# Optimization experiments

Hardware: AMD Instinct MI355X
Metric: run time of the kernel (lower is better)

## Reference

```python
import jax, jax.numpy as jnp
import numpy as np

B, L = 128, 5000
D_MODEL, N_LAYERS, D_STATE, D_INNER, D_CONV, DT_RANK = 8, 4, 16, 16, 3, 1
HID, N_CLASSES = 64, 230


def setup_inputs():
    key = jax.random.key(0)
    ks = iter(jax.random.split(key, 32))
    nrm = lambda shape, s=0.02: jax.random.normal(next(ks), shape, jnp.float32) * s
    return {
        "x": jax.random.uniform(next(ks), (B, L), jnp.float32),
        "idx": jnp.arange(L, dtype=jnp.int32),
        "embed": nrm((L, D_MODEL), 1.0),
        "norm_w": jnp.ones((N_LAYERS, D_MODEL), jnp.float32),
        "in_proj_w": nrm((N_LAYERS, 2 * D_INNER, D_MODEL), 0.2),
        "conv_w": nrm((N_LAYERS, D_INNER, 1, D_CONV), 0.3),
        "conv_b": nrm((N_LAYERS, D_INNER)),
        "x_proj_w": nrm((N_LAYERS, DT_RANK + 2 * D_STATE, D_INNER), 0.2),
        "dt_proj_w": nrm((N_LAYERS, D_INNER, DT_RANK), 0.5),
        "dt_proj_b": nrm((N_LAYERS, D_INNER), 0.1),
        "A_log": jnp.broadcast_to(jnp.log(jnp.arange(1., D_STATE + 1.)), (N_LAYERS, D_INNER, D_STATE)).astype(jnp.float32),
        "Dp": jnp.ones((N_LAYERS, D_INNER), jnp.float32),
        "out_proj_w": nrm((N_LAYERS, D_MODEL, D_INNER), 0.2),
        "c1_w": nrm((HID, D_MODEL, 3), 0.2), "c1_b": nrm((HID,)),
        "c2_w": nrm((HID, HID, 3), 0.1), "c2_b": nrm((HID,)),
        "c3_w": nrm((HID, HID, 3), 0.1), "c3_b": nrm((HID,)),
        "fc_w": nrm((N_CLASSES, HID), 0.1), "fc_b": jnp.zeros((N_CLASSES,), jnp.float32),
    }


def _conv1d(x, w, b, pad, groups=1):
    # x: [B, C, L], w: [O, I/groups, K]
    y = jax.lax.conv_general_dilated(x, w, (1,), [pad], dimension_numbers=("NCH", "OIH", "NCH"), feature_group_count=groups)
    return y + b[None, :, None]


def _rmsnorm(x, w, eps=1e-5):
    return x * jax.lax.rsqrt(jnp.mean(x * x, -1, keepdims=True) + eps) * w


def _selective_scan(u, delta, A, Bm, Cm, Dv):
    # u, delta: [B, L, ED]; A: [ED, N]; Bm, Cm: [B, L, N]
    dA = jnp.exp(delta[..., None] * A)                       # [B, L, ED, N]
    dBu = delta[..., None] * Bm[:, :, None, :] * u[..., None]  # [B, L, ED, N]

    def step(h, t):
        dA_t, dBu_t, c_t = t
        h = dA_t * h + dBu_t                                  # [B, ED, N]
        return h, jnp.einsum("ben,bn->be", h, c_t)

    h0 = jnp.zeros((dA.shape[0], dA.shape[2], dA.shape[3]), u.dtype)
    _, ys = jax.lax.scan(step, h0, (dA.swapaxes(0, 1), dBu.swapaxes(0, 1), Cm.swapaxes(0, 1)))
    return ys.swapaxes(0, 1) + Dv * u


def reference(x, idx, embed, norm_w, in_proj_w, conv_w, conv_b, x_proj_w, dt_proj_w, dt_proj_b, A_log, Dp, out_proj_w, c1_w, c1_b, c2_w, c2_b, c3_w, c3_b, fc_w, fc_b):
    # embedding(idx) broadcast over batch, gated by intensities x
    f = embed[idx][None, :, :] * x[:, :, None]                # [B, L, D_MODEL]
    for l in range(N_LAYERS):
        xn = _rmsnorm(f, norm_w[l])
        xz = xn @ in_proj_w[l].T                              # [B, L, 2*ED]
        xc, z = xz[..., :D_INNER], xz[..., D_INNER:]
        xc = _conv1d(xc.swapaxes(1, 2), conv_w[l], conv_b[l], (D_CONV - 1, 0), D_INNER).swapaxes(1, 2)
        xc = jax.nn.silu(xc)
        dbc = xc @ x_proj_w[l].T                              # [B, L, dt_rank+2N]
        delta = jax.nn.softplus(dbc[..., :DT_RANK] @ dt_proj_w[l].T + dt_proj_b[l])
        Bm = dbc[..., DT_RANK:DT_RANK + D_STATE]
        Cm = dbc[..., DT_RANK + D_STATE:]
        y = _selective_scan(xc, delta, -jnp.exp(A_log[l]), Bm, Cm, Dp[l])
        f = (y * jax.nn.silu(z)) @ out_proj_w[l].T + f        # residual
    feat = f.swapaxes(1, 2)                                   # [B, D_MODEL, L]
    h = jax.nn.relu(_conv1d(feat, c1_w, c1_b, (1, 1)))
    r = jax.nn.relu(_conv1d(h, c2_w, c2_b, (1, 1)))
    r = _conv1d(r, c3_w, c3_b, (1, 1))
    h = jax.nn.relu(h + r)                                    # residual conv block
    pooled = h.mean(-1)                                       # [B, HID]
    return pooled @ fc_w.T + fc_b                             # [B, N_CLASSES]
```

## Files before the change

kernel.cpp:

```cpp
#include <hip/hip_runtime.h>
#include <math.h>

#define B 128
#define L 5000
#define NL 4
#define NCH 50
#define LC 100
#define ST 50
#define HT 128

typedef __attribute__((ext_vector_type(8))) short bf16x8;
typedef __attribute__((ext_vector_type(4))) short short4v;
typedef __attribute__((ext_vector_type(4))) float f32x4;

__device__ __forceinline__ float sigmoidf_(float x){ return 1.f/(1.f+__expf(-x)); }
__device__ __forceinline__ float siluf_(float x){ return x*sigmoidf_(x); }
__device__ __forceinline__ float softplusf_(float x){ return fmaxf(x,0.f) + log1pf(__expf(-fabsf(x))); }
__device__ __forceinline__ short bfc_(float x){
  union { float f; unsigned u; } v; v.f = x;
  unsigned r = v.u + 0x7fffu + ((v.u >> 16) & 1u);
  return (short)(r >> 16);
}
__device__ __forceinline__ float b2f_(short s){
  union { unsigned u; float f; } v; v.u = ((unsigned)(unsigned short)s) << 16;
  return v.f;
}
#define SW(row, col) (((row)<<6) + ((col) ^ (((row)&7)<<3)))

__global__ void k_embed(const float* __restrict__ x, const int* __restrict__ idx,
                        const float* __restrict__ embed, float* __restrict__ f){
  int gid = blockIdx.x*256 + threadIdx.x;
  if (gid >= B*L) return;
  int t = gid % L;
  float xv = x[gid];
  const float* er = embed + (size_t)idx[t]*8;
  float4 e0 = *(const float4*)(er);
  float4 e1 = *(const float4*)(er+4);
  *(float4*)(f + (size_t)gid*8)   = make_float4(e0.x*xv, e0.y*xv, e0.z*xv, e0.w*xv);
  *(float4*)(f + (size_t)gid*8+4) = make_float4(e1.x*xv, e1.y*xv, e1.z*xv, e1.w*xv);
}

__global__ __launch_bounds__(256,4) void k_l1(const float* __restrict__ fin,
    const float* __restrict__ norm_w, const float* __restrict__ in_proj,
    const float* __restrict__ conv_w, const float* __restrict__ conv_b,
    const float* __restrict__ x_proj, const float* __restrict__ dt_w,
    const float* __restrict__ dt_b, const float* __restrict__ A_log,
    float* __restrict__ Sc, float* __restrict__ Pc,
    float2* __restrict__ duA, float2* __restrict__ BCA, float* __restrict__ szA){
  __shared__ float fsub[52][8], rn[52];
  __shared__ float uL[ST][17];
  __shared__ float2 duL[ST][16];
  __shared__ float BLs[ST][17];
  __shared__ float dbc0[ST];
  int tid = threadIdx.x, ch = blockIdx.x, b = blockIdx.y;
  int e = tid>>4, n = tid&15;
  int ct = tid&15;
  float ipnw_c[8], ipnwz_c[8], cwc[3];
  #pragma unroll
  for (int d=0;d<8;d++){
    ipnw_c[d]  = in_proj[ct*8+d]*norm_w[d];
    ipnwz_c[d] = in_proj[(16+ct)*8+d]*norm_w[d];
  }
  #pragma unroll
  for (int k=0;k<3;k++) cwc[k] = conv_w[ct*3+k];
  float cbc = conv_b[ct];
  float xp0_c = x_proj[ct];
  float xpB_r[16], xpC_r[16];
  #pragma unroll
  for (int k=0;k<16;k++){
    xpB_r[k] = x_proj[(1+ct)*16+k];
    xpC_r[k] = x_proj[(17+ct)*16+k];
  }
  float dtw_e = dt_w[ct], dtb_e = dt_b[ct];
  float a = -__expf(A_log[e*16+n]);
  float h = 0.f, dsum = 0.f;
  int t00 = ch*LC;
  for (int sub=0; sub<LC/ST; sub++){
    int ts = t00 + sub*ST;
    __syncthreads();
    for (int i=tid;i<104;i+=256){ int r=i>>1, half=i&1; int t=ts-2+r;
      *(float4*)&fsub[r][half*4] = (t>=0) ? *(const float4*)&fin[((size_t)b*L+t)*8+half*4]
                                          : make_float4(0.f,0.f,0.f,0.f); }
    __syncthreads();
    if (tid < 52){ float ss=0.f;
      #pragma unroll
      for (int d=0;d<8;d++){ float v=fsub[tid][d]; ss += v*v; }
      rn[tid] = rsqrtf(ss*0.125f + 1e-5f); }
    __syncthreads();
    for (int i=tid;i<ST*16;i+=256){ int j=i>>4;
      float acc = cbc;
      #pragma unroll
      for (int kk=0;kk<3;kk++){
        int r = j + kk;
        float dot=0.f;
        #pragma unroll
        for (int d=0;d<8;d++) dot += ipnw_c[d]*fsub[r][d];
        acc += cwc[kk]*(dot*rn[r]);
      }
      float uv = siluf_(acc);
      uL[j][ct] = uv;
      int r2 = j + 2;
      float dz=0.f;
      #pragma unroll
      for (int d=0;d<8;d++) dz += ipnwz_c[d]*fsub[r2][d];
      szA[((size_t)b*L + ts + j)*16 + ct] = siluf_(dz*rn[r2]);
      float pp = xp0_c*uv;
      pp += __shfl_xor(pp, 1, 64);
      pp += __shfl_xor(pp, 2, 64);
      pp += __shfl_xor(pp, 4, 64);
      pp += __shfl_xor(pp, 8, 64);
      if (ct == 0) dbc0[j] = pp;
    }
    __syncthreads();
    for (int i=tid;i<ST*16;i+=256){ int j=i>>4;
      float accB=0.f, accC=0.f;
      #pragma unroll
      for (int c=0;c<16;c++){
        float uv2 = uL[j][c];
        accB += xpB_r[c]*uv2;
        accC += xpC_r[c]*uv2;
      }
      BLs[j][ct] = accB;
      float dd = softplusf_(dbc0[j]*dtw_e + dtb_e);
      float uv = uL[j][ct];
      duL[j][ct] = make_float2(dd, dd*uv);
      size_t gi = ((size_t)b*L + ts + j)*16 + ct;
      BCA[gi] = make_float2(accB, accC);
      duA[gi] = make_float2(dd, uv);
    }
    __syncthreads();
    for (int j=0;j<ST;j++){
      float2 du = duL[j][e];
      float bb = BLs[j][n];
      h = __expf(du.x*a)*h + du.y*bb;
      dsum += du.x;
    }
  }
  size_t o = ((size_t)b*NCH + ch)*256 + tid;
  Sc[o] = h;
  Pc[o] = __expf(a*dsum);
}

__global__ __launch_bounds__(256,4) void k_l3(const float* __restrict__ fin, float* __restrict__ fout,
    const float* __restrict__ A_log, const float* __restrict__ Dp,
    const float* __restrict__ Sc, const float* __restrict__ Pc,
    const float* __restrict__ ow,
    const float2* __restrict__ duA, const float2* __restrict__ BCA,
    const float* __restrict__ szA){
  __shared__ float2 duL[ST*16], BCL[ST*16];
  __shared__ float uLs[ST*16], szL[ST*16], yL[ST*16];
  __shared__ float hcL[10*320];
  __shared__ float s_owp[8*17], s_De[16];
  int tid = threadIdx.x, ch = blockIdx.x, b = blockIdx.y;
  int e = tid>>4, n = tid&15;
  int dt8 = tid&7;
  float a = -__expf(A_log[e*16+n]);
  if (tid < 128) s_owp[(tid>>4)*17 + (tid&15)] = ow[tid];
  if (tid < 16) s_De[tid] = Dp[tid];
  float h = 0.f;
  for (int c2=0; c2<ch; c2++){
    size_t o = ((size_t)b*NCH + c2)*256 + tid;
    h = Pc[o]*h + Sc[o];
  }
  int t00 = ch*LC;
  for (int sub=0; sub<LC/ST; sub++){
    int ts = t00 + sub*ST;
    __syncthreads();
    const f32x4* duG = (const f32x4*)(duA + ((size_t)b*L + ts)*16);
    const f32x4* bcG = (const f32x4*)(BCA + ((size_t)b*L + ts)*16);
    for (int i=tid;i<400;i+=256){
      f32x4 v = duG[i];
      int bidx = i*2;
      duL[bidx]   = make_float2(v[0], v[0]*v[1]);
      duL[bidx+1] = make_float2(v[2], v[2]*v[3]);
      uLs[bidx]   = v[1];
      uLs[bidx+1] = v[3];
      f32x4 wv = bcG[i];
      BCL[bidx]   = make_float2(wv[0], wv[1]);
      BCL[bidx+1] = make_float2(wv[2], wv[3]);
    }
    const f32x4* szG = (const f32x4*)(szA + ((size_t)b*L + ts)*16);
    for (int i=tid;i<200;i+=256){
      *(f32x4*)&szL[i*4] = szG[i];
    }
    __syncthreads();
    for (int q=0; q<ST/10; q++){
      #pragma unroll
      for (int j2=0; j2<10; j2++){
        int j = q*10 + j2;
        float2 du = duL[j*16+e];
        float2 bc = BCL[j*16+n];
        h = __expf(du.x*a)*h + du.y*bc.x;
        hcL[j2*320 + e*20 + n] = h*bc.y;
      }
      __syncthreads();
      if (tid < 160){
        int jj = tid>>4, ee = tid&15;
        int j = q*10 + jj;
        const f32x4* hp = (const f32x4*)&hcL[jj*320 + ee*20];
        f32x4 p0 = hp[0], p1 = hp[1], p2 = hp[2], p3 = hp[3];
        float s = ((p0[0]+p0[1])+(p0[2]+p0[3])) + ((p1[0]+p1[1])+(p1[2]+p1[3]))
                + ((p2[0]+p2[1])+(p2[2]+p2[3])) + ((p3[0]+p3[1])+(p3[2]+p3[3]));
        yL[j*16+ee] = (s + s_De[ee]*uLs[j*16+ee]) * szL[j*16+ee];
      }
      __syncthreads();
    }
    for (int i=tid;i<ST*8;i+=256){ int j=i>>3;
      size_t fi = ((size_t)b*L + ts + j)*8 + dt8;
      float acc = fin[fi];
      f32x4 y0 = *(const f32x4*)&yL[j*16];
      f32x4 y1 = *(const f32x4*)&yL[j*16+4];
      f32x4 y2 = *(const f32x4*)&yL[j*16+8];
      f32x4 y3 = *(const f32x4*)&yL[j*16+12];
      #pragma unroll
      for (int c=0;c<4;c++)
        acc += s_owp[dt8*17+c]*y0[c] + s_owp[dt8*17+4+c]*y1[c]
             + s_owp[dt8*17+8+c]*y2[c] + s_owp[dt8*17+12+c]*y3[c];
      fout[fi] = acc;
    }
  }
}

__global__ void k_wt(const float* __restrict__ c1w, const float* __restrict__ c2w,
                     const float* __restrict__ c3w, short* __restrict__ wt1b,
                     short* __restrict__ wt2b, short* __restrict__ wt3b){
  int idx = blockIdx.x*256 + threadIdx.x;
  if (idx < 2048){
    int c = idx >> 5, m = idx & 31;
    int kk = m >> 3, d = m & 7;
    wt1b[idx] = (kk < 3) ? bfc_(c1w[c*24 + d*3 + kk]) : (short)0;
  } else if (idx < 2048 + 12288){
    int i = idx - 2048;
    int c = i / 192, rem = i % 192;
    int k = rem >> 6, ci = rem & 63;
    wt2b[i] = bfc_(c2w[c*192 + ci*3 + k]);
  } else if (idx < 2048 + 24576){
    int i = idx - 2048 - 12288;
    int c = i / 192, rem = i % 192;
    int k = rem >> 6, ci = rem & 63;
    wt3b[i] = bfc_(c3w[c*192 + ci*3 + k]);
  }
}

__global__ __launch_bounds__(256) void k_head(const float* __restrict__ f,
   const short* __restrict__ wt1b, const float* __restrict__ c1b,
   const short* __restrict__ wt2b, const float* __restrict__ c2b,
   const short* __restrict__ wt3b, const float* __restrict__ c3b,
   float* __restrict__ pooled){
  __shared__ short fs_b[146*8];
  __shared__ short h1t[146*64];
  __shared__ short h2t[130*64];
  int tid  = threadIdx.x;
  int b    = blockIdx.y;
  int t0   = blockIdx.x * HT;
  int lane = tid & 63;
  int w    = tid >> 6;
  int cb   = w*16;
  int lc   = lane & 15, g = lane >> 4;

  for (int task = tid; task < 146*8; task += 256){
    int r = task >> 3, d = task & 7;
    int t = t0 - 3 + r;
    float v = (r < 134 && t >= 0 && t < L) ? f[((size_t)b*L + t)*8 + d] : 0.f;
    fs_b[task] = bfc_(v);
  }
  for (int i = tid; i < 14*64; i += 256){
    int row = 132 + (i>>6), col = i&63;
    h1t[SW(row, col)] = 0;
  }
  __syncthreads();

  {
    bf16x8 a1 = *(const bf16x8*)(wt1b + (cb + lc)*32 + g*8);
    f32x4 bias1 = *(const f32x4*)(c1b + cb + (g<<2));
    #pragma unroll
    for (int nt=0; nt<9; nt++){
      int tcol = nt*16 + lc;
      bf16x8 bv = {0,0,0,0,0,0,0,0};
      if (g < 3) bv = *(bf16x8*)&fs_b[(tcol+g)*8];
      f32x4 acc = {0.f,0.f,0.f,0.f};
      acc = __builtin_amdgcn_mfma_f32_16x16x32_bf16(a1, bv, acc, 0, 0, 0);
      if (tcol < 132){
        int t1 = t0 - 2 + tcol;
        bool v = (t1 >= 0 && t1 < L);
        short4v pk;
        #pragma unroll
        for (int reg=0;reg<4;reg++)
          pk[reg] = bfc_(v ? fmaxf(acc[reg] + bias1[reg], 0.f) : 0.f);
        *(short4v*)&h1t[SW(tcol, cb + (g<<2))] = pk;
      }
    }
  }
  __syncthreads();

  {
    const short* wA = wt2b + (cb + lc)*192 + g*8;
    bf16x8 a2[6];
    #pragma unroll
    for (int s=0;s<6;s++) a2[s] = *(const bf16x8*)(wA + 32*s);
    f32x4 bias2 = *(const f32x4*)(c2b + cb + (g<<2));
    #pragma unroll
    for (int nt=0; nt<9; nt++){
      f32x4 acc = {0.f,0.f,0.f,0.f};
      #pragma unroll
      for (int s=0;s<6;s++){
        int k = s>>1, ci0 = (s&1)*32;
        int jr = nt*16 + lc + k;
        bf16x8 bfr = *(bf16x8*)&h1t[SW(jr, ci0 + g*8)];
        acc = __builtin_amdgcn_mfma_f32_16x16x32_bf16(a2[s], bfr, acc, 0, 0, 0);
      }
      int tr = nt*16 + lc;
      if (tr < 130){
        int tg = t0 - 1 + tr;
        bool v = (tg >= 0 && tg < L);
        short4v pk;
        #pragma unroll
        for (int reg=0;reg<4;reg++)
          pk[reg] = bfc_(v ? fmaxf(acc[reg] + bias2[reg], 0.f) : 0.f);
        *(short4v*)&h2t[SW(tr, cb + (g<<2))] = pk;
      }
    }
  }
  __syncthreads();

  {
    const short* wA = wt3b + (cb + lc)*192 + g*8;
    bf16x8 a3[6];
    #pragma unroll
    for (int s=0;s<6;s++) a3[s] = *(const bf16x8*)(wA + 32*s);
    f32x4 bias3 = *(const f32x4*)(c3b + cb + (g<<2));
    int c0 = cb + (g<<2);
    float pool[4] = {0.f,0.f,0.f,0.f};
    #pragma unroll
    for (int nt=0; nt<8; nt++){
      f32x4 acc = {0.f,0.f,0.f,0.f};
      #pragma unroll
      for (int s=0;s<6;s++){
        int k = s>>1, ci0 = (s&1)*32;
        int jr = nt*16 + lc + k;
        bf16x8 bfr = *(bf16x8*)&h2t[SW(jr, ci0 + g*8)];
        acc = __builtin_amdgcn_mfma_f32_16x16x32_bf16(a3[s], bfr, acc, 0, 0, 0);
      }
      int t = t0 + nt*16 + lc;
      short4v hres = *(short4v*)&h1t[SW(nt*16 + lc + 2, c0)];
      if (t < L){
        #pragma unroll
        for (int reg=0;reg<4;reg++)
          pool[reg] += fmaxf(b2f_(hres[reg]) + acc[reg] + bias3[reg], 0.f);
      }
    }
    #pragma unroll
    for (int m=1; m<16; m<<=1){
      #pragma unroll
      for (int reg=0;reg<4;reg++) pool[reg] += __shfl_xor(pool[reg], m, 64);
    }
    if (lc == 0){
      #pragma unroll
      for (int reg=0;reg<4;reg++) atomicAdd(&pooled[b*64 + c0 + reg], pool[reg]);
    }
  }
}

__global__ void k_fc(const float* __restrict__ pooled, const float* __restrict__ fcw,
                     const float* __restrict__ fcb, float* __restrict__ out){
  int gid = blockIdx.x*256 + threadIdx.x;
  if (gid >= B*230) return;
  int b = gid / 230, j = gid % 230;
  const float* p = pooled + b*64;
  const float* wv = fcw + j*64;
  float a = 0.f;
  #pragma unroll
  for (int c=0;c<64;c++) a += p[c]*wv[c];
  out[gid] = a*(1.f/(float)L) + fcb[j];
}

extern "C" void kernel_launch(void* const* d_in, const int* in_sizes, int n_in,
                              void* d_out, int out_size, void* d_ws, size_t ws_size,
                              hipStream_t stream){
  const float* x      = (const float*)d_in[0];
  const int*   idx    = (const int*)  d_in[1];
  const float* embed  = (const float*)d_in[2];
  const float* norm_w = (const float*)d_in[3];
  const float* in_proj= (const float*)d_in[4];
  const float* conv_w = (const float*)d_in[5];
  const float* conv_b = (const float*)d_in[6];
  const float* x_proj = (const float*)d_in[7];
  const float* dt_w   = (const float*)d_in[8];
  const float* dt_b   = (const float*)d_in[9];
  const float* A_log  = (const float*)d_in[10];
  const float* Dp     = (const float*)d_in[11];
  const float* out_w  = (const float*)d_in[12];
  const float* c1w    = (const float*)d_in[13];
  const float* c1b    = (const float*)d_in[14];
  const float* c2w    = (const float*)d_in[15];
  const float* c2b    = (const float*)d_in[16];
  const float* c3w    = (const float*)d_in[17];
  const float* c3b    = (const float*)d_in[18];
  const float* fcw    = (const float*)d_in[19];
  const float* fcb    = (const float*)d_in[20];
  float* out = (float*)d_out;

  float* ws = (float*)d_ws;
  float* f0     = ws;
  float* f1     = f0 + 5120000;
  float* Sc     = f1 + 5120000;
  float* Pc     = Sc + 1638400;
  float* pooled = Pc + 1638400;
  float2* duA   = (float2*)(pooled + 8192);
  float2* BCA   = duA + 10240000;
  float* szA    = (float*)(BCA + 10240000);
  short* wt1b   = (short*)(szA + 10240000);
  short* wt2b   = wt1b + 2048;
  short* wt3b   = wt2b + 12288;

  k_wt<<<104,256,0,stream>>>(c1w, c2w, c3w, wt1b, wt2b, wt3b);
  k_embed<<<2500,256,0,stream>>>(x, idx, embed, f0);
  for (int l=0;l<NL;l++){
    const float* fin = (l & 1) ? f1 : f0;
    float*       fo  = (l & 1) ? f0 : f1;
    k_l1<<<dim3(NCH,B),256,0,stream>>>(fin, norm_w + l*8, in_proj + l*256, conv_w + l*48,
         conv_b + l*16, x_proj + l*528, dt_w + l*16, dt_b + l*16, A_log + l*256,
         Sc, Pc, duA, BCA, szA);
    k_l3<<<dim3(NCH,B),256,0,stream>>>(fin, fo, A_log + l*256, Dp + l*16, Sc, Pc,
         out_w + l*128, duA, BCA, szA);
  }
  (void)hipMemsetAsync(pooled, 0, B*64*sizeof(float), stream);
  k_head<<<dim3((L+HT-1)/HT,B),256,0,stream>>>(f0, wt1b, c1b, wt2b, c2b, wt3b, c3b, pooled);
  k_fc<<<(B*230+255)/256,256,0,stream>>>(pooled, fcw, fcb, out);
}
```

Measured before the change: 1.146 ms.

## Precompute chunk prefix states and replace LDS reduction with wave shuffles

Adds a small kernel that runs the cross-chunk carry recurrence once per batch and writes each chunk's starting state, replacing the O(chunk index) serial prefix loop every k_l3 block used to run. Inside k_l3, the per-step reduction over the 16 state lanes now uses __shfl_xor butterflies instead of an LDS staging buffer with two barriers per group. This drops barriers and LDS traffic but adds a kernel launch and serializes 50 chunks per batch in a 128-block kernel.

```diff
diff --git a/kernel.cpp b/kernel.cpp
--- a/kernel.cpp
+++ b/kernel.cpp
@@ -141,15 +141,24 @@
   Pc[o] = __expf(a*dsum);
 }
 
+__global__ __launch_bounds__(256) void k_p2(float* __restrict__ Sc, const float* __restrict__ Pc){
+  int tid = threadIdx.x, b = blockIdx.x;
+  float h = 0.f;
+  for (int ch=0; ch<NCH; ch++){
+    size_t o = ((size_t)b*NCH + ch)*256 + tid;
+    float s = Sc[o], pc = Pc[o];
+    Sc[o] = h;
+    h = pc*h + s;
+  }
+}
+
 __global__ __launch_bounds__(256,4) void k_l3(const float* __restrict__ fin, float* __restrict__ fout,
     const float* __restrict__ A_log, const float* __restrict__ Dp,
-    const float* __restrict__ Sc, const float* __restrict__ Pc,
-    const float* __restrict__ ow,
+    const float* __restrict__ h0A, const float* __restrict__ ow,
     const float2* __restrict__ duA, const float2* __restrict__ BCA,
     const float* __restrict__ szA){
   __shared__ float2 duL[ST*16], BCL[ST*16];
   __shared__ float uLs[ST*16], szL[ST*16], yL[ST*16];
-  __shared__ float hcL[10*320];
   __shared__ float s_owp[8*17], s_De[16];
   int tid = threadIdx.x, ch = blockIdx.x, b = blockIdx.y;
   int e = tid>>4, n = tid&15;
@@ -157,15 +166,11 @@
   float a = -__expf(A_log[e*16+n]);
   if (tid < 128) s_owp[(tid>>4)*17 + (tid&15)] = ow[tid];
   if (tid < 16) s_De[tid] = Dp[tid];
-  float h = 0.f;
-  for (int c2=0; c2<ch; c2++){
-    size_t o = ((size_t)b*NCH + c2)*256 + tid;
-    h = Pc[o]*h + Sc[o];
-  }
+  float h = h0A[((size_t)b*NCH + ch)*256 + tid];
+  float De_e = Dp[e];
   int t00 = ch*LC;
   for (int sub=0; sub<LC/ST; sub++){
     int ts = t00 + sub*ST;
-    __syncthreads();
     const f32x4* duG = (const f32x4*)(duA + ((size_t)b*L + ts)*16);
     const f32x4* bcG = (const f32x4*)(BCA + ((size_t)b*L + ts)*16);
     for (int i=tid;i<400;i+=256){
@@ -185,26 +190,31 @@
     }
     __syncthreads();
     for (int q=0; q<ST/10; q++){
+      float p[10];
       #pragma unroll
       for (int j2=0; j2<10; j2++){
         int j = q*10 + j2;
         float2 du = duL[j*16+e];
         float2 bc = BCL[j*16+n];
         h = __expf(du.x*a)*h + du.y*bc.x;
-        hcL[j2*320 + e*20 + n] = h*bc.y;
-      }
-      __syncthreads();
-      if (tid < 160){
-        int jj = tid>>4, ee = tid&15;
-        int j = q*10 + jj;
-        const f32x4* hp = (const f32x4*)&hcL[jj*320 + ee*20];
-        f32x4 p0 = hp[0], p1 = hp[1], p2 = hp[2], p3 = hp[3];
-        float s = ((p0[0]+p0[1])+(p0[2]+p0[3])) + ((p1[0]+p1[1])+(p1[2]+p1[3]))
-                + ((p2[0]+p2[1])+(p2[2]+p2[3])) + ((p3[0]+p3[1])+(p3[2]+p3[3]));
-        yL[j*16+ee] = (s + s_De[ee]*uLs[j*16+ee]) * szL[j*16+ee];
-      }
-      __syncthreads();
-    }
+        p[j2] = h*bc.y;
+      }
+      #pragma unroll
+      for (int j2=0; j2<10; j2++){
+        p[j2] += __shfl_xor(p[j2], 1, 64);
+        p[j2] += __shfl_xor(p[j2], 2, 64);
+        p[j2] += __shfl_xor(p[j2], 4, 64);
+        p[j2] += __shfl_xor(p[j2], 8, 64);
+      }
+      if (n == 0){
+        #pragma unroll
+        for (int j2=0; j2<10; j2++){
+          int j = q*10 + j2;
+          yL[j*16+e] = (p[j2] + De_e*uLs[j*16+e]) * szL[j*16+e];
+        }
+      }
+    }
+    __syncthreads();
     for (int i=tid;i<ST*8;i+=256){ int j=i>>3;
       size_t fi = ((size_t)b*L + ts + j)*8 + dt8;
       float acc = fin[fi];
@@ -218,6 +228,7 @@
              + s_owp[dt8*17+8+c]*y2[c] + s_owp[dt8*17+12+c]*y3[c];
       fout[fi] = acc;
     }
+    __syncthreads();
   }
 }
 
@@ -421,7 +432,8 @@
     k_l1<<<dim3(NCH,B),256,0,stream>>>(fin, norm_w + l*8, in_proj + l*256, conv_w + l*48,
          conv_b + l*16, x_proj + l*528, dt_w + l*16, dt_b + l*16, A_log + l*256,
          Sc, Pc, duA, BCA, szA);
-    k_l3<<<dim3(NCH,B),256,0,stream>>>(fin, fo, A_log + l*256, Dp + l*16, Sc, Pc,
+    k_p2<<<B,256,0,stream>>>(Sc, Pc);
+    k_l3<<<dim3(NCH,B),256,0,stream>>>(fin, fo, A_log + l*256, Dp + l*16, Sc,
          out_w + l*128, duA, BCA, szA);
   }
   (void)hipMemsetAsync(pooled, 0, B*64*sizeof(float), stream);
```

Result: slower. 1.360 ms (+18.6%).
